# Optimization experiments

Measured on AMD Instinct MI355X. Metric: run time of the kernel, lower is better.

## Reference

```python
import jax, jax.numpy as jnp
import numpy as np

LOG2 = 0.6931471805599453

def ssp(x):
    # shifted softplus, SchNet's standard activation
    return jax.nn.softplus(x) - LOG2

def setup_inputs() -> dict:
    key = jax.random.key(0)
    ks = jax.random.split(key, 8)
    B, A, N, G, F = 8, 1024, 64, 50, 128
    s = lambda fan_in: 1.0 / np.sqrt(fan_in)
    return {
        "x": jax.random.normal(ks[0], (B, A, F), jnp.float32),
        "pairwise_mask": jnp.ones((B, A, N), jnp.float32),
        "neighbors": jax.random.randint(ks[1], (B, A, N), 0, A),
        "f_ij": jax.random.uniform(ks[2], (B, A, N, G), jnp.float32),
        "W_f1": jax.random.normal(ks[3], (G, F), jnp.float32) * s(G),
        "b_f1": jnp.zeros((F,), jnp.float32),
        "W_f2": jax.random.normal(ks[4], (F, F), jnp.float32) * s(F),
        "b_f2": jnp.zeros((F,), jnp.float32),
        "W_in2f": jax.random.normal(ks[5], (F, F), jnp.float32) * s(F),
        "W_f2out": jax.random.normal(ks[6], (F, F), jnp.float32) * s(F),
        "b_f2out": jnp.zeros((F,), jnp.float32),
    }

def reference(x, pairwise_mask, neighbors, f_ij, W_f1, b_f1, W_f2, b_f2,
              W_in2f, W_f2out, b_f2out):
    B, A, N = neighbors.shape
    # filter network: Dense+ssp then Dense (no activation) -> [B,A,N,F]
    W = ssp(jnp.einsum('bang,gf->banf', f_ij, W_f1) + b_f1)
    W = jnp.einsum('banf,fk->bank', W, W_f2) + b_f2
    # neighbor gather: x[b, neighbors[b,a,n], :] -> [B,A,N,C]
    nbh = neighbors.reshape(B, A * N, 1)           # [B, A*N, 1]
    x_nbh = jnp.take_along_axis(x, nbh, axis=1)    # broadcast over C -> [B, A*N, C]
    x_nbh = x_nbh.reshape(B, A, N, -1)
    # in2f dense (no bias), filter multiply, masked sum over neighbor axis
    y = jnp.einsum('banc,cf->banf', x_nbh, W_in2f)
    y = y * W
    y = jnp.sum(y * pairwise_mask[..., None], axis=2)  # [B, A, F]
    # f2out dense with shifted-softplus activation
    y = ssp(jnp.einsum('baf,fo->bao', y, W_f2out) + b_f2out)
    return y
```

## Files before the change

### kernel.cpp

```cpp
#include <hip/hip_runtime.h>

#define B_ 8
#define A_ 1024
#define N_ 64
#define G_ 50
#define F_ 128
#define ATOMS 4

typedef __attribute__((ext_vector_type(8))) short bf16x8;
typedef __attribute__((ext_vector_type(4))) float f32x4;

__device__ __forceinline__ float sspf(float v) {
    return __logf(1.f + __expf(v)) - 0.69314718055994530942f;
}
__device__ __forceinline__ float ssp2(float v) {
    return __log2f(1.f + exp2f(v)) - 1.f;
}
__device__ __forceinline__ unsigned short f2bf(float f) {
    unsigned u = __float_as_uint(f);
    u += 0x7fffu + ((u >> 16) & 1u);
    return (unsigned short)(u >> 16);
}
__device__ __forceinline__ unsigned cvt_pk(float lo, float hi) {
    unsigned r;
    asm("v_cvt_pk_bf16_f32 %0, %1, %2" : "=v"(r) : "v"(lo), "v"(hi));
    return r;
}
template <int CTRL>
__device__ __forceinline__ float dppadd(float v) {
    int x = __builtin_amdgcn_mov_dpp(__float_as_int(v), CTRL, 0xF, 0xF, true);
    return v + __int_as_float(x);
}
__device__ __forceinline__ float red16(float p) {
    p = dppadd<0xB1>(p);
    p = dppadd<0x4E>(p);
    p = dppadd<0x141>(p);
    p = dppadd<0x140>(p);
    return p;
}

__global__ __launch_bounds__(256) void pack_all(
    const float* __restrict__ W1, const float* __restrict__ b1,
    const float* __restrict__ W2, const float* __restrict__ Wi,
    const float* __restrict__ Wo,
    unsigned short* __restrict__ P1, unsigned short* __restrict__ P2,
    unsigned short* __restrict__ Pi, unsigned short* __restrict__ Po)
{
    int blk = blockIdx.x;
    const float* W; const float* bias = nullptr; unsigned short* P; int K, id;
    float scale;
    if (blk < 32)       { W = W1; P = P1; K = 50;  id = blk * 256 + threadIdx.x; bias = b1;
                          scale = 1.44269504088896340736f; }
    else if (blk < 96)  { W = W2; P = P2; K = 128; id = (blk - 32) * 256 + threadIdx.x;
                          scale = 0.69314718055994530942f; }
    else if (blk < 160) { W = Wi; P = Pi; K = 128; id = (blk - 96) * 256 + threadIdx.x;
                          scale = 1.f; }
    else                { W = Wo; P = Po; K = 128; id = (blk - 160) * 256 + threadIdx.x;
                          scale = 1.f; }
    int i    = id & 7;
    int lane = (id >> 3) & 63;
    int nt   = (id >> 9) & 7;
    int ks   = id >> 12;
    int k = 32 * ks + 8 * (lane >> 4) + i;
    int f = 16 * nt + (lane & 15);
    float v = (k < K) ? W[k * F_ + f] : ((bias && k == K) ? bias[f] : 0.f);
    P[id] = f2bf(scale * v);
}

template <bool ACT, bool OUT_BF16>
__global__ __launch_bounds__(64) void rowgemm_kernel(
    const float* Afp, const unsigned short* __restrict__ Bp,
    const float* __restrict__ bias, void* outv)
{
    const int l  = threadIdx.x;
    const int r0 = blockIdx.x * 16;
    const bf16x8* Bv = (const bf16x8*)Bp;

    f32x4 acc[8];
    #pragma unroll
    for (int nt = 0; nt < 8; ++nt) acc[nt] = f32x4{0.f, 0.f, 0.f, 0.f};

    const int arow = r0 + (l & 15);
    const int koff = (l >> 4) * 8;
    #pragma unroll
    for (int ks = 0; ks < 4; ++ks) {
        const float* ap = Afp + (size_t)arow * F_ + ks * 32 + koff;
        float4 a0 = *(const float4*)ap;
        float4 a1 = *(const float4*)(ap + 4);
        bf16x8 af;
        af[0] = (short)f2bf(a0.x); af[1] = (short)f2bf(a0.y);
        af[2] = (short)f2bf(a0.z); af[3] = (short)f2bf(a0.w);
        af[4] = (short)f2bf(a1.x); af[5] = (short)f2bf(a1.y);
        af[6] = (short)f2bf(a1.z); af[7] = (short)f2bf(a1.w);
        #pragma unroll
        for (int nt = 0; nt < 8; ++nt) {
            bf16x8 bf = Bv[(ks * 8 + nt) * 64 + l];
            acc[nt] = __builtin_amdgcn_mfma_f32_16x16x32_bf16(af, bf, acc[nt], 0, 0, 0);
        }
    }
    #pragma unroll
    for (int nt = 0; nt < 8; ++nt) {
        int f = nt * 16 + (l & 15);
        float bv = bias ? bias[f] : 0.f;
        #pragma unroll
        for (int r = 0; r < 4; ++r) {
            int orow = r0 + (l >> 4) * 4 + r;
            float v = acc[nt][r] + bv;
            if (ACT) v = sspf(v);
            if (OUT_BF16) ((unsigned short*)outv)[(size_t)orow * F_ + f] = f2bf(v);
            else          ((float*)outv)[(size_t)orow * F_ + f] = v;
        }
    }
}

__global__ __launch_bounds__(256, 3) void cfconv_main(
    const unsigned short* __restrict__ xt,
    const float* __restrict__ mask,
    const int*   __restrict__ nbr,
    const float* __restrict__ fij,
    const unsigned short* __restrict__ W1s,
    const unsigned short* __restrict__ W2s,
    const float* __restrict__ bf2,
    float* __restrict__ Y)
{
    const int bid = blockIdx.x;
    const int swz = (bid & 7) * (2048 / 8) + (bid >> 3);
    const int ba0 = swz * ATOMS;
    const int t   = threadIdx.x;
    const int w   = t >> 6;
    const int l   = t & 63;
    const int l16 = l & 15;
    const int q   = l >> 4;

    __shared__ unsigned short s_fp[2][4096];
    __shared__ unsigned short s_hp[2][8192];

    const unsigned short* xt_b = xt + ((size_t)(ba0 >> 10) << 10) * F_;
    const int xoff = 32 * w + 4 * q;

    const bf16x8* w1v = (const bf16x8*)W1s;
    const bf16x8* w2v = (const bf16x8*)W2s;
    bf16x8 W1r[2][2], W2r[4][2];
    #pragma unroll
    for (int ks = 0; ks < 2; ++ks) {
        W1r[ks][0] = w1v[(ks * 8 + 2 * w + 0) * 64 + l];
        W1r[ks][1] = w1v[(ks * 8 + 2 * w + 1) * 64 + l];
    }
    #pragma unroll
    for (int ks = 0; ks < 4; ++ks) {
        W2r[ks][0] = w2v[(ks * 8 + 2 * w + 0) * 64 + l];
        W2r[ks][1] = w2v[(ks * 8 + 2 * w + 1) * 64 + l];
    }
    f32x4 b2acc[2];
    {
        float4 t0 = *(const float4*)(bf2 + 16 * (2 * w + 0) + 4 * q);
        float4 t1 = *(const float4*)(bf2 + 16 * (2 * w + 1) + 4 * q);
        b2acc[0] = f32x4{t0.x, t0.y, t0.z, t0.w};
        b2acc[1] = f32x4{t1.x, t1.y, t1.z, t1.w};
    }

    int nbv[4]; float mkv[4];
    {
        const int*   nb0 = nbr  + (size_t)ba0 * N_;
        const float* mk0 = mask + (size_t)ba0 * N_;
        #pragma unroll
        for (int nt = 0; nt < 4; ++nt) {
            nbv[nt] = nb0[16 * nt + l16];
            mkv[nt] = mk0[16 * nt + l16];
        }
    }
    float2 fa[4], fb[4];
    {
        const float* frow = fij + (size_t)ba0 * (N_ * G_) + (16 * w + l16) * G_;
        #pragma unroll
        for (int j = 0; j < 4; ++j) fa[j] = *(const float2*)(frow + 8 * q + 2 * j);
        if (q < 2) {
            #pragma unroll
            for (int j = 0; j < 4; ++j) fb[j] = *(const float2*)(frow + 32 + 8 * q + 2 * j);
        } else if (q == 2) {
            fb[0] = *(const float2*)(frow + 48);
            fb[1] = float2{1.f, 0.f};
            fb[2] = float2{0.f, 0.f}; fb[3] = float2{0.f, 0.f};
        } else {
            #pragma unroll
            for (int j = 0; j < 4; ++j) fb[j] = float2{0.f, 0.f};
        }
    }
    uint2 xg[2][4];
    #pragma unroll
    for (int f2 = 0; f2 < 2; ++f2)
        #pragma unroll
        for (int nt = 0; nt < 4; ++nt)
            xg[f2][nt] = *(const uint2*)(xt_b + nbv[nt] * F_ + xoff + 16 * f2);
    {
        uint4 pk0, pk1;
        pk0.x = cvt_pk(fa[0].x, fa[0].y); pk0.y = cvt_pk(fa[1].x, fa[1].y);
        pk0.z = cvt_pk(fa[2].x, fa[2].y); pk0.w = cvt_pk(fa[3].x, fa[3].y);
        pk1.x = cvt_pk(fb[0].x, fb[0].y); pk1.y = cvt_pk(fb[1].x, fb[1].y);
        pk1.z = cvt_pk(fb[2].x, fb[2].y); pk1.w = cvt_pk(fb[3].x, fb[3].y);
        *(uint4*)(&s_fp[0][((w * 2 + 0) * 64 + l) * 8]) = pk0;
        *(uint4*)(&s_fp[0][((w * 2 + 1) * 64 + l) * 8]) = pk1;
    }
    __syncthreads();

    int nbv2[4]; float mkv2[4];

    #pragma unroll
    for (int i = 0; i < ATOMS; ++i) {
        const int ba = ba0 + i;
        const bf16x8* fv = (const bf16x8*)s_fp[i & 1];
        unsigned short* fp_nxt = s_fp[(i + 1) & 1];
        unsigned short* hp_cur = s_hp[i & 1];

        f32x4 acc1[2][4];
        __builtin_amdgcn_s_setprio(1);
        {
            bf16x8 bb[4];
            #pragma unroll
            for (int nt = 0; nt < 4; ++nt) bb[nt] = fv[(nt * 2 + 0) * 64 + l];
            #pragma unroll
            for (int nt = 0; nt < 4; ++nt) {
                acc1[0][nt] = __builtin_amdgcn_mfma_f32_16x16x32_bf16(W1r[0][0], bb[nt], f32x4{0.f,0.f,0.f,0.f}, 0, 0, 0);
                acc1[1][nt] = __builtin_amdgcn_mfma_f32_16x16x32_bf16(W1r[0][1], bb[nt], f32x4{0.f,0.f,0.f,0.f}, 0, 0, 0);
            }
            #pragma unroll
            for (int nt = 0; nt < 4; ++nt) bb[nt] = fv[(nt * 2 + 1) * 64 + l];
            #pragma unroll
            for (int nt = 0; nt < 4; ++nt) {
                acc1[0][nt] = __builtin_amdgcn_mfma_f32_16x16x32_bf16(W1r[1][0], bb[nt], acc1[0][nt], 0, 0, 0);
                acc1[1][nt] = __builtin_amdgcn_mfma_f32_16x16x32_bf16(W1r[1][1], bb[nt], acc1[1][nt], 0, 0, 0);
            }
        }
        __builtin_amdgcn_s_setprio(0);

        if (i < ATOMS - 1) {
            const float* frow = fij + (size_t)(ba + 1) * (N_ * G_) + (16 * w + l16) * G_;
            #pragma unroll
            for (int j = 0; j < 4; ++j) fa[j] = *(const float2*)(frow + 8 * q + 2 * j);
            if (q < 2) {
                #pragma unroll
                for (int j = 0; j < 4; ++j) fb[j] = *(const float2*)(frow + 32 + 8 * q + 2 * j);
            } else if (q == 2) {
                fb[0] = *(const float2*)(frow + 48);
                fb[1] = float2{1.f, 0.f};
                fb[2] = float2{0.f, 0.f}; fb[3] = float2{0.f, 0.f};
            } else {
                #pragma unroll
                for (int j = 0; j < 4; ++j) fb[j] = float2{0.f, 0.f};
            }
            const int*   nb1 = nbr  + (size_t)(ba + 1) * N_;
            const float* mk1 = mask + (size_t)(ba + 1) * N_;
            #pragma unroll
            for (int nt = 0; nt < 4; ++nt) {
                nbv2[nt] = nb1[16 * nt + l16];
                mkv2[nt] = mk1[16 * nt + l16];
            }
        }

        #pragma unroll
        for (int ct2 = 0; ct2 < 2; ++ct2) {
            const int addr = ((w * 64 + 16 * (2 * ct2 + (q >> 1)) + l16) * 8 + 4 * (q & 1));
            #pragma unroll
            for (int nt = 0; nt < 4; ++nt) {
                float h0 = ssp2(acc1[ct2][nt][0]);
                float h1 = ssp2(acc1[ct2][nt][1]);
                float h2 = ssp2(acc1[ct2][nt][2]);
                float h3 = ssp2(acc1[ct2][nt][3]);
                uint2 pk;
                pk.x = cvt_pk(h0, h1);
                pk.y = cvt_pk(h2, h3);
                *(uint2*)(&hp_cur[nt * 2048 + addr]) = pk;
            }
        }

        if (i < ATOMS - 1) {
            uint4 pk0, pk1;
            pk0.x = cvt_pk(fa[0].x, fa[0].y); pk0.y = cvt_pk(fa[1].x, fa[1].y);
            pk0.z = cvt_pk(fa[2].x, fa[2].y); pk0.w = cvt_pk(fa[3].x, fa[3].y);
            pk1.x = cvt_pk(fb[0].x, fb[0].y); pk1.y = cvt_pk(fb[1].x, fb[1].y);
            pk1.z = cvt_pk(fb[2].x, fb[2].y); pk1.w = cvt_pk(fb[3].x, fb[3].y);
            *(uint4*)(&fp_nxt[((w * 2 + 0) * 64 + l) * 8]) = pk0;
            *(uint4*)(&fp_nxt[((w * 2 + 1) * 64 + l) * 8]) = pk1;
        }
        __syncthreads();

        const bf16x8* hv = (const bf16x8*)hp_cur;
        f32x4 acc2[2][4];
        __builtin_amdgcn_s_setprio(1);
        {
            bf16x8 bb[4];
            #pragma unroll
            for (int nt = 0; nt < 4; ++nt) bb[nt] = hv[(nt * 4 + 0) * 64 + l];
            #pragma unroll
            for (int nt = 0; nt < 4; ++nt) {
                acc2[0][nt] = __builtin_amdgcn_mfma_f32_16x16x32_bf16(W2r[0][0], bb[nt], b2acc[0], 0, 0, 0);
                acc2[1][nt] = __builtin_amdgcn_mfma_f32_16x16x32_bf16(W2r[0][1], bb[nt], b2acc[1], 0, 0, 0);
            }
            #pragma unroll
            for (int ks = 1; ks < 4; ++ks) {
                #pragma unroll
                for (int nt = 0; nt < 4; ++nt) bb[nt] = hv[(nt * 4 + ks) * 64 + l];
                #pragma unroll
                for (int nt = 0; nt < 4; ++nt) {
                    acc2[0][nt] = __builtin_amdgcn_mfma_f32_16x16x32_bf16(W2r[ks][0], bb[nt], acc2[0][nt], 0, 0, 0);
                    acc2[1][nt] = __builtin_amdgcn_mfma_f32_16x16x32_bf16(W2r[ks][1], bb[nt], acc2[1][nt], 0, 0, 0);
                }
            }
        }
        __builtin_amdgcn_s_setprio(0);

        #pragma unroll
        for (int f2 = 0; f2 < 2; ++f2) {
            float p0 = 0.f, p1 = 0.f, p2 = 0.f, p3 = 0.f;
            #pragma unroll
            for (int nt = 0; nt < 4; ++nt) {
                const float msk = mkv[nt];
                const uint2 xv = xg[f2][nt];
                const float x0 = __uint_as_float(xv.x << 16);
                const float x1 = __uint_as_float(xv.x & 0xffff0000u);
                const float x2 = __uint_as_float(xv.y << 16);
                const float x3 = __uint_as_float(xv.y & 0xffff0000u);
                p0 = fmaf(msk * acc2[f2][nt][0], x0, p0);
                p1 = fmaf(msk * acc2[f2][nt][1], x1, p1);
                p2 = fmaf(msk * acc2[f2][nt][2], x2, p2);
                p3 = fmaf(msk * acc2[f2][nt][3], x3, p3);
            }
            p0 = red16(p0); p1 = red16(p1); p2 = red16(p2); p3 = red16(p3);
            if (l16 == 0)
                *(float4*)(Y + (size_t)ba * F_ + 16 * (2 * w + f2) + 4 * q) = float4{p0, p1, p2, p3};
        }

        if (i < ATOMS - 1) {
            #pragma unroll
            for (int nt = 0; nt < 4; ++nt) { nbv[nt] = nbv2[nt]; mkv[nt] = mkv2[nt]; }
            #pragma unroll
            for (int f2 = 0; f2 < 2; ++f2)
                #pragma unroll
                for (int nt = 0; nt < 4; ++nt)
                    xg[f2][nt] = *(const uint2*)(xt_b + nbv[nt] * F_ + xoff + 16 * f2);
        }
    }
}

extern "C" void kernel_launch(void* const* d_in, const int* in_sizes, int n_in,
                              void* d_out, int out_size, void* d_ws, size_t ws_size,
                              hipStream_t stream) {
    const float* x     = (const float*)d_in[0];
    const float* mask  = (const float*)d_in[1];
    const int*   nbr   = (const int*)d_in[2];
    const float* fij   = (const float*)d_in[3];
    const float* Wf1   = (const float*)d_in[4];
    const float* bf1   = (const float*)d_in[5];
    const float* Wf2   = (const float*)d_in[6];
    const float* bf2   = (const float*)d_in[7];
    const float* Win2f = (const float*)d_in[8];
    const float* Wout  = (const float*)d_in[9];
    const float* bout  = (const float*)d_in[10];
    float* out = (float*)d_out;

    char* ws = (char*)d_ws;
    unsigned short* W1p   = (unsigned short*)(ws);
    unsigned short* W2p   = (unsigned short*)(ws + 16384);
    unsigned short* Winp  = (unsigned short*)(ws + 49152);
    unsigned short* Woutp = (unsigned short*)(ws + 81920);
    unsigned short* xt    = (unsigned short*)(ws + 114688);

    pack_all<<<224, 256, 0, stream>>>(Wf1, bf1, Wf2, Win2f, Wout, W1p, W2p, Winp, Woutp);

    rowgemm_kernel<false, true><<<B_ * A_ / 16, 64, 0, stream>>>(x, Winp, nullptr, xt);

    cfconv_main<<<B_ * A_ / ATOMS, 256, 0, stream>>>(xt, mask, nbr, fij, W1p, W2p, bf2, out);

    rowgemm_kernel<true, false><<<B_ * A_ / 16, 64, 0, stream>>>(out, Woutp, bout, out);
}
```

Before: 77.80 us.

## Split cfconv work across 8 waves with one 16-column feature tile each

```diff
diff --git a/kernel.cpp b/kernel.cpp
--- a/kernel.cpp
+++ b/kernel.cpp
@@ -113,7 +113,7 @@
     }
 }
 
-__global__ __launch_bounds__(256, 3) void cfconv_main(
+__global__ __launch_bounds__(512, 4) void cfconv_main(
     const unsigned short* __restrict__ xt,
     const float* __restrict__ mask,
     const int*   __restrict__ nbr,
@@ -131,32 +131,26 @@
     const int l   = t & 63;
     const int l16 = l & 15;
     const int q   = l >> 4;
+    const int mt  = w >> 1;
+    const int ksf = w & 1;
 
     __shared__ unsigned short s_fp[2][4096];
     __shared__ unsigned short s_hp[2][8192];
 
     const unsigned short* xt_b = xt + ((size_t)(ba0 >> 10) << 10) * F_;
-    const int xoff = 32 * w + 4 * q;
+    const int xoff = 16 * w + 4 * q;
 
     const bf16x8* w1v = (const bf16x8*)W1s;
     const bf16x8* w2v = (const bf16x8*)W2s;
-    bf16x8 W1r[2][2], W2r[4][2];
-    #pragma unroll
-    for (int ks = 0; ks < 2; ++ks) {
-        W1r[ks][0] = w1v[(ks * 8 + 2 * w + 0) * 64 + l];
-        W1r[ks][1] = w1v[(ks * 8 + 2 * w + 1) * 64 + l];
-    }
-    #pragma unroll
-    for (int ks = 0; ks < 4; ++ks) {
-        W2r[ks][0] = w2v[(ks * 8 + 2 * w + 0) * 64 + l];
-        W2r[ks][1] = w2v[(ks * 8 + 2 * w + 1) * 64 + l];
-    }
-    f32x4 b2acc[2];
+    bf16x8 W1r[2], W2r[4];
+    #pragma unroll
+    for (int ks = 0; ks < 2; ++ks) W1r[ks] = w1v[(ks * 8 + w) * 64 + l];
+    #pragma unroll
+    for (int ks = 0; ks < 4; ++ks) W2r[ks] = w2v[(ks * 8 + w) * 64 + l];
+    f32x4 b2acc;
     {
-        float4 t0 = *(const float4*)(bf2 + 16 * (2 * w + 0) + 4 * q);
-        float4 t1 = *(const float4*)(bf2 + 16 * (2 * w + 1) + 4 * q);
-        b2acc[0] = f32x4{t0.x, t0.y, t0.z, t0.w};
-        b2acc[1] = f32x4{t1.x, t1.y, t1.z, t1.w};
+        float4 t0 = *(const float4*)(bf2 + xoff);
+        b2acc = f32x4{t0.x, t0.y, t0.z, t0.w};
     }
 
     int nbv[4]; float mkv[4];
@@ -169,41 +163,38 @@
             mkv[nt] = mk0[16 * nt + l16];
         }
     }
-    float2 fa[4], fb[4];
+    float2 fa[4];
     {
-        const float* frow = fij + (size_t)ba0 * (N_ * G_) + (16 * w + l16) * G_;
-        #pragma unroll
-        for (int j = 0; j < 4; ++j) fa[j] = *(const float2*)(frow + 8 * q + 2 * j);
-        if (q < 2) {
-            #pragma unroll
-            for (int j = 0; j < 4; ++j) fb[j] = *(const float2*)(frow + 32 + 8 * q + 2 * j);
+        const float* frow = fij + (size_t)ba0 * (N_ * G_) + (16 * mt + l16) * G_;
+        if (ksf == 0) {
+            #pragma unroll
+            for (int j = 0; j < 4; ++j) fa[j] = *(const float2*)(frow + 8 * q + 2 * j);
+        } else if (q < 2) {
+            #pragma unroll
+            for (int j = 0; j < 4; ++j) fa[j] = *(const float2*)(frow + 32 + 8 * q + 2 * j);
         } else if (q == 2) {
-            fb[0] = *(const float2*)(frow + 48);
-            fb[1] = float2{1.f, 0.f};
-            fb[2] = float2{0.f, 0.f}; fb[3] = float2{0.f, 0.f};
+            fa[0] = *(const float2*)(frow + 48);
+            fa[1] = float2{1.f, 0.f};
+            fa[2] = float2{0.f, 0.f}; fa[3] = float2{0.f, 0.f};
         } else {
             #pragma unroll
-            for (int j = 0; j < 4; ++j) fb[j] = float2{0.f, 0.f};
-        }
-    }
-    uint2 xg[2][4];
-    #pragma unroll
-    for (int f2 = 0; f2 < 2; ++f2)
-        #pragma unroll
-        for (int nt = 0; nt < 4; ++nt)
-            xg[f2][nt] = *(const uint2*)(xt_b + nbv[nt] * F_ + xoff + 16 * f2);
+            for (int j = 0; j < 4; ++j) fa[j] = float2{0.f, 0.f};
+        }
+    }
+    uint2 xg[4];
+    #pragma unroll
+    for (int nt = 0; nt < 4; ++nt)
+        xg[nt] = *(const uint2*)(xt_b + nbv[nt] * F_ + xoff);
     {
-        uint4 pk0, pk1;
-        pk0.x = cvt_pk(fa[0].x, fa[0].y); pk0.y = cvt_pk(fa[1].x, fa[1].y);
-        pk0.z = cvt_pk(fa[2].x, fa[2].y); pk0.w = cvt_pk(fa[3].x, fa[3].y);
-        pk1.x = cvt_pk(fb[0].x, fb[0].y); pk1.y = cvt_pk(fb[1].x, fb[1].y);
-        pk1.z = cvt_pk(fb[2].x, fb[2].y); pk1.w = cvt_pk(fb[3].x, fb[3].y);
-        *(uint4*)(&s_fp[0][((w * 2 + 0) * 64 + l) * 8]) = pk0;
-        *(uint4*)(&s_fp[0][((w * 2 + 1) * 64 + l) * 8]) = pk1;
+        uint4 pk;
+        pk.x = cvt_pk(fa[0].x, fa[0].y); pk.y = cvt_pk(fa[1].x, fa[1].y);
+        pk.z = cvt_pk(fa[2].x, fa[2].y); pk.w = cvt_pk(fa[3].x, fa[3].y);
+        *(uint4*)(&s_fp[0][(w * 64 + l) * 8]) = pk;
     }
     __syncthreads();
 
     int nbv2[4]; float mkv2[4];
+    const int haddr = ((w >> 1) * 64 + 16 * ((2 * w + (q >> 1)) & 3) + l16) * 8 + 4 * (q & 1);
 
     #pragma unroll
     for (int i = 0; i < ATOMS; ++i) {
@@ -212,41 +203,38 @@
         unsigned short* fp_nxt = s_fp[(i + 1) & 1];
         unsigned short* hp_cur = s_hp[i & 1];
 
-        f32x4 acc1[2][4];
+        f32x4 acc1[4];
         __builtin_amdgcn_s_setprio(1);
         {
             bf16x8 bb[4];
             #pragma unroll
             for (int nt = 0; nt < 4; ++nt) bb[nt] = fv[(nt * 2 + 0) * 64 + l];
             #pragma unroll
-            for (int nt = 0; nt < 4; ++nt) {
-                acc1[0][nt] = __builtin_amdgcn_mfma_f32_16x16x32_bf16(W1r[0][0], bb[nt], f32x4{0.f,0.f,0.f,0.f}, 0, 0, 0);
-                acc1[1][nt] = __builtin_amdgcn_mfma_f32_16x16x32_bf16(W1r[0][1], bb[nt], f32x4{0.f,0.f,0.f,0.f}, 0, 0, 0);
-            }
+            for (int nt = 0; nt < 4; ++nt)
+                acc1[nt] = __builtin_amdgcn_mfma_f32_16x16x32_bf16(W1r[0], bb[nt], f32x4{0.f,0.f,0.f,0.f}, 0, 0, 0);
             #pragma unroll
             for (int nt = 0; nt < 4; ++nt) bb[nt] = fv[(nt * 2 + 1) * 64 + l];
             #pragma unroll
-            for (int nt = 0; nt < 4; ++nt) {
-                acc1[0][nt] = __builtin_amdgcn_mfma_f32_16x16x32_bf16(W1r[1][0], bb[nt], acc1[0][nt], 0, 0, 0);
-                acc1[1][nt] = __builtin_amdgcn_mfma_f32_16x16x32_bf16(W1r[1][1], bb[nt], acc1[1][nt], 0, 0, 0);
-            }
+            for (int nt = 0; nt < 4; ++nt)
+                acc1[nt] = __builtin_amdgcn_mfma_f32_16x16x32_bf16(W1r[1], bb[nt], acc1[nt], 0, 0, 0);
         }
         __builtin_amdgcn_s_setprio(0);
 
         if (i < ATOMS - 1) {
-            const float* frow = fij + (size_t)(ba + 1) * (N_ * G_) + (16 * w + l16) * G_;
-            #pragma unroll
-            for (int j = 0; j < 4; ++j) fa[j] = *(const float2*)(frow + 8 * q + 2 * j);
-            if (q < 2) {
-                #pragma unroll
-                for (int j = 0; j < 4; ++j) fb[j] = *(const float2*)(frow + 32 + 8 * q + 2 * j);
+            const float* frow = fij + (size_t)(ba + 1) * (N_ * G_) + (16 * mt + l16) * G_;
+            if (ksf == 0) {
+                #pragma unroll
+                for (int j = 0; j < 4; ++j) fa[j] = *(const float2*)(frow + 8 * q + 2 * j);
+            } else if (q < 2) {
+                #pragma unroll
+                for (int j = 0; j < 4; ++j) fa[j] = *(const float2*)(frow + 32 + 8 * q + 2 * j);
             } else if (q == 2) {
-                fb[0] = *(const float2*)(frow + 48);
-                fb[1] = float2{1.f, 0.f};
-                fb[2] = float2{0.f, 0.f}; fb[3] = float2{0.f, 0.f};
+                fa[0] = *(const float2*)(frow + 48);
+                fa[1] = float2{1.f, 0.f};
+                fa[2] = float2{0.f, 0.f}; fa[3] = float2{0.f, 0.f};
             } else {
                 #pragma unroll
-                for (int j = 0; j < 4; ++j) fb[j] = float2{0.f, 0.f};
+                for (int j = 0; j < 4; ++j) fa[j] = float2{0.f, 0.f};
             }
             const int*   nb1 = nbr  + (size_t)(ba + 1) * N_;
             const float* mk1 = mask + (size_t)(ba + 1) * N_;
@@ -258,86 +246,72 @@
         }
 
         #pragma unroll
-        for (int ct2 = 0; ct2 < 2; ++ct2) {
-            const int addr = ((w * 64 + 16 * (2 * ct2 + (q >> 1)) + l16) * 8 + 4 * (q & 1));
-            #pragma unroll
-            for (int nt = 0; nt < 4; ++nt) {
-                float h0 = ssp2(acc1[ct2][nt][0]);
-                float h1 = ssp2(acc1[ct2][nt][1]);
-                float h2 = ssp2(acc1[ct2][nt][2]);
-                float h3 = ssp2(acc1[ct2][nt][3]);
-                uint2 pk;
-                pk.x = cvt_pk(h0, h1);
-                pk.y = cvt_pk(h2, h3);
-                *(uint2*)(&hp_cur[nt * 2048 + addr]) = pk;
-            }
+        for (int nt = 0; nt < 4; ++nt) {
+            float h0 = ssp2(acc1[nt][0]);
+            float h1 = ssp2(acc1[nt][1]);
+            float h2 = ssp2(acc1[nt][2]);
+            float h3 = ssp2(acc1[nt][3]);
+            uint2 pk;
+            pk.x = cvt_pk(h0, h1);
+            pk.y = cvt_pk(h2, h3);
+            *(uint2*)(&hp_cur[nt * 2048 + haddr]) = pk;
         }
 
         if (i < ATOMS - 1) {
-            uint4 pk0, pk1;
-            pk0.x = cvt_pk(fa[0].x, fa[0].y); pk0.y = cvt_pk(fa[1].x, fa[1].y);
-            pk0.z = cvt_pk(fa[2].x, fa[2].y); pk0.w = cvt_pk(fa[3].x, fa[3].y);
-            pk1.x = cvt_pk(fb[0].x, fb[0].y); pk1.y = cvt_pk(fb[1].x, fb[1].y);
-            pk1.z = cvt_pk(fb[2].x, fb[2].y); pk1.w = cvt_pk(fb[3].x, fb[3].y);
-            *(uint4*)(&fp_nxt[((w * 2 + 0) * 64 + l) * 8]) = pk0;
-            *(uint4*)(&fp_nxt[((w * 2 + 1) * 64 + l) * 8]) = pk1;
+            uint4 pk;
+            pk.x = cvt_pk(fa[0].x, fa[0].y); pk.y = cvt_pk(fa[1].x, fa[1].y);
+            pk.z = cvt_pk(fa[2].x, fa[2].y); pk.w = cvt_pk(fa[3].x, fa[3].y);
+            *(uint4*)(&fp_nxt[(w * 64 + l) * 8]) = pk;
         }
         __syncthreads();
 
         const bf16x8* hv = (const bf16x8*)hp_cur;
-        f32x4 acc2[2][4];
+        f32x4 acc2[4];
         __builtin_amdgcn_s_setprio(1);
         {
             bf16x8 bb[4];
             #pragma unroll
             for (int nt = 0; nt < 4; ++nt) bb[nt] = hv[(nt * 4 + 0) * 64 + l];
             #pragma unroll
-            for (int nt = 0; nt < 4; ++nt) {
-                acc2[0][nt] = __builtin_amdgcn_mfma_f32_16x16x32_bf16(W2r[0][0], bb[nt], b2acc[0], 0, 0, 0);
-                acc2[1][nt] = __builtin_amdgcn_mfma_f32_16x16x32_bf16(W2r[0][1], bb[nt], b2acc[1], 0, 0, 0);
+            for (int nt = 0; nt < 4; ++nt)
+                acc2[nt] = __builtin_amdgcn_mfma_f32_16x16x32_bf16(W2r[0], bb[nt], b2acc, 0, 0, 0);
+            #pragma unroll
+            for (int ks = 1; ks < 4; ++ks) {
+                #pragma unroll
+                for (int nt = 0; nt < 4; ++nt) bb[nt] = hv[(nt * 4 + ks) * 64 + l];
+                #pragma unroll
+                for (int nt = 0; nt < 4; ++nt)
+                    acc2[nt] = __builtin_amdgcn_mfma_f32_16x16x32_bf16(W2r[ks], bb[nt], acc2[nt], 0, 0, 0);
             }
-            #pragma unroll
-            for (int ks = 1; ks < 4; ++ks) {
-                #pragma unroll
-                for (int nt = 0; nt < 4; ++nt) bb[nt] = hv[(nt * 4 + ks) * 64 + l];
-                #pragma unroll
-                for (int nt = 0; nt < 4; ++nt) {
-                    acc2[0][nt] = __builtin_amdgcn_mfma_f32_16x16x32_bf16(W2r[ks][0], bb[nt], acc2[0][nt], 0, 0, 0);
-                    acc2[1][nt] = __builtin_amdgcn_mfma_f32_16x16x32_bf16(W2r[ks][1], bb[nt], acc2[1][nt], 0, 0, 0);
-                }
-            }
         }
         __builtin_amdgcn_s_setprio(0);
 
-        #pragma unroll
-        for (int f2 = 0; f2 < 2; ++f2) {
+        {
             float p0 = 0.f, p1 = 0.f, p2 = 0.f, p3 = 0.f;
             #pragma unroll
             for (int nt = 0; nt < 4; ++nt) {
                 const float msk = mkv[nt];
-                const uint2 xv = xg[f2][nt];
+                const uint2 xv = xg[nt];
                 const float x0 = __uint_as_float(xv.x << 16);
                 const float x1 = __uint_as_float(xv.x & 0xffff0000u);
                 const float x2 = __uint_as_float(xv.y << 16);
                 const float x3 = __uint_as_float(xv.y & 0xffff0000u);
-                p0 = fmaf(msk * acc2[f2][nt][0], x0, p0);
-                p1 = fmaf(msk * acc2[f2][nt][1], x1, p1);
-                p2 = fmaf(msk * acc2[f2][nt][2], x2, p2);
-                p3 = fmaf(msk * acc2[f2][nt][3], x3, p3);
+                p0 = fmaf(msk * acc2[nt][0], x0, p0);
+                p1 = fmaf(msk * acc2[nt][1], x1, p1);
+                p2 = fmaf(msk * acc2[nt][2], x2, p2);
+                p3 = fmaf(msk * acc2[nt][3], x3, p3);
             }
             p0 = red16(p0); p1 = red16(p1); p2 = red16(p2); p3 = red16(p3);
             if (l16 == 0)
-                *(float4*)(Y + (size_t)ba * F_ + 16 * (2 * w + f2) + 4 * q) = float4{p0, p1, p2, p3};
+                *(float4*)(Y + (size_t)ba * F_ + xoff) = float4{p0, p1, p2, p3};
         }
 
         if (i < ATOMS - 1) {
             #pragma unroll
             for (int nt = 0; nt < 4; ++nt) { nbv[nt] = nbv2[nt]; mkv[nt] = mkv2[nt]; }
             #pragma unroll
-            for (int f2 = 0; f2 < 2; ++f2)
-                #pragma unroll
-                for (int nt = 0; nt < 4; ++nt)
-                    xg[f2][nt] = *(const uint2*)(xt_b + nbv[nt] * F_ + xoff + 16 * f2);
+            for (int nt = 0; nt < 4; ++nt)
+                xg[nt] = *(const uint2*)(xt_b + nbv[nt] * F_ + xoff);
         }
     }
 }
@@ -369,7 +343,7 @@
 
     rowgemm_kernel<false, true><<<B_ * A_ / 16, 64, 0, stream>>>(x, Winp, nullptr, xt);
 
-    cfconv_main<<<B_ * A_ / ATOMS, 256, 0, stream>>>(xt, mask, nbr, fij, W1p, W2p, bf2, out);
+    cfconv_main<<<B_ * A_ / ATOMS, 512, 0, stream>>>(xt, mask, nbr, fij, W1p, W2p, bf2, out);
 
     rowgemm_kernel<true, false><<<B_ * A_ / 16, 64, 0, stream>>>(out, Woutp, bout, out);
 }
```

Measured after the change: 80.99 us. +4.1%, slower.

## Fuse f2out dense and shifted-softplus epilogue into cfconv main kernel

Applied to the files above, without the earlier changes.

```diff
diff --git a/kernel.cpp b/kernel.cpp
--- a/kernel.cpp
+++ b/kernel.cpp
@@ -121,7 +121,9 @@
     const unsigned short* __restrict__ W1s,
     const unsigned short* __restrict__ W2s,
     const float* __restrict__ bf2,
-    float* __restrict__ Y)
+    const unsigned short* __restrict__ Wouts,
+    const float* __restrict__ bout,
+    float* __restrict__ out)
 {
     const int bid = blockIdx.x;
     const int swz = (bid & 7) * (2048 / 8) + (bid >> 3);
@@ -134,6 +136,7 @@
 
     __shared__ unsigned short s_fp[2][4096];
     __shared__ unsigned short s_hp[2][8192];
+    __shared__ float s_Y[ATOMS][F_];
 
     const unsigned short* xt_b = xt + ((size_t)(ba0 >> 10) << 10) * F_;
     const int xoff = 32 * w + 4 * q;
@@ -327,17 +330,59 @@
             }
             p0 = red16(p0); p1 = red16(p1); p2 = red16(p2); p3 = red16(p3);
             if (l16 == 0)
-                *(float4*)(Y + (size_t)ba * F_ + 16 * (2 * w + f2) + 4 * q) = float4{p0, p1, p2, p3};
+                *(float4*)(&s_Y[i][16 * (2 * w + f2) + 4 * q]) = float4{p0, p1, p2, p3};
         }
 
         if (i < ATOMS - 1) {
             #pragma unroll
             for (int nt = 0; nt < 4; ++nt) { nbv[nt] = nbv2[nt]; mkv[nt] = mkv2[nt]; }
             #pragma unroll
-            for (int f2 = 0; f2 < 2; ++f2)
-                #pragma unroll
-                for (int nt = 0; nt < 4; ++nt)
-                    xg[f2][nt] = *(const uint2*)(xt_b + nbv[nt] * F_ + xoff + 16 * f2);
+            for (int nt = 0; nt < 4; ++nt) {
+                xg[0][nt] = *(const uint2*)(xt_b + nbv[nt] * F_ + xoff);
+                xg[1][nt] = *(const uint2*)(xt_b + nbv[nt] * F_ + xoff + 16);
+            }
+        }
+    }
+    __syncthreads();
+
+    {
+        const bf16x8* wov = (const bf16x8*)Wouts;
+        bf16x8 WOr0[4], WOr1[4];
+        #pragma unroll
+        for (int ks = 0; ks < 4; ++ks) {
+            WOr0[ks] = wov[(ks * 8 + 2 * w + 0) * 64 + l];
+            WOr1[ks] = wov[(ks * 8 + 2 * w + 1) * 64 + l];
+        }
+        f32x4 acc3[2];
+        {
+            float4 t0 = *(const float4*)(bout + 16 * (2 * w + 0) + 4 * q);
+            float4 t1 = *(const float4*)(bout + 16 * (2 * w + 1) + 4 * q);
+            acc3[0] = f32x4{t0.x, t0.y, t0.z, t0.w};
+            acc3[1] = f32x4{t1.x, t1.y, t1.z, t1.w};
+        }
+        const int yr = l16 & 3;
+        #pragma unroll
+        for (int ks = 0; ks < 4; ++ks) {
+            const float* yp = &s_Y[yr][ks * 32 + q * 8];
+            float4 y0 = *(const float4*)yp;
+            float4 y1 = *(const float4*)(yp + 4);
+            uint4 u;
+            u.x = cvt_pk(y0.x, y0.y); u.y = cvt_pk(y0.z, y0.w);
+            u.z = cvt_pk(y1.x, y1.y); u.w = cvt_pk(y1.z, y1.w);
+            bf16x8 yb = *(bf16x8*)&u;
+            acc3[0] = __builtin_amdgcn_mfma_f32_16x16x32_bf16(WOr0[ks], yb, acc3[0], 0, 0, 0);
+            acc3[1] = __builtin_amdgcn_mfma_f32_16x16x32_bf16(WOr1[ks], yb, acc3[1], 0, 0, 0);
+        }
+        if (l16 < ATOMS) {
+            float* orow = out + (size_t)(ba0 + l16) * F_;
+            #pragma unroll
+            for (int ct2 = 0; ct2 < 2; ++ct2) {
+                float o0 = sspf(acc3[ct2][0]);
+                float o1 = sspf(acc3[ct2][1]);
+                float o2 = sspf(acc3[ct2][2]);
+                float o3 = sspf(acc3[ct2][3]);
+                *(float4*)(orow + 16 * (2 * w + ct2) + 4 * q) = float4{o0, o1, o2, o3};
+            }
         }
     }
 }
@@ -369,7 +414,6 @@
 
     rowgemm_kernel<false, true><<<B_ * A_ / 16, 64, 0, stream>>>(x, Winp, nullptr, xt);
 
-    cfconv_main<<<B_ * A_ / ATOMS, 256, 0, stream>>>(xt, mask, nbr, fij, W1p, W2p, bf2, out);
-
-    rowgemm_kernel<true, false><<<B_ * A_ / 16, 64, 0, stream>>>(out, Woutp, bout, out);
-}
+    cfconv_main<<<B_ * A_ / ATOMS, 256, 0, stream>>>(xt, mask, nbr, fij, W1p, W2p, bf2,
+                                                     Woutp, bout, out);
+}
```

Measured after the change: 78.74 us. No clear change (+1.2%).
